# Kernel tuning notes

Hardware: AMD Instinct MI355X
Metric: run time of the kernel (lower is better)

## Reference

```python
import jax, jax.numpy as jnp
import numpy as np

V, CV, F, E, H, A, CD = 10000, 64, 2048, 512, 512, 512, 128
B, LCAP = 128, 31  # 30 decode steps


def setup_inputs() -> dict:
    key = jax.random.key(0)
    ks = jax.random.split(key, 24)
    g = lambda k, shp, s: (jax.random.normal(k, shp, jnp.float32) * s)
    return {
        "att_feats": g(ks[0], (B, F, 7, 7), 1.0),
        "fc_feats": g(ks[1], (B, F), 1.0),
        "captions": jax.random.randint(ks[2], (B, LCAP), 0, V),
        "count_vecs": g(ks[3], (B, CV), 1.0),
        "embed_w": jax.random.uniform(ks[4], (V, E), jnp.float32, -0.1, 0.1),
        "cm_w1": g(ks[5], (CD, CV), 0.05), "cm_b1": jnp.zeros((CD,), jnp.float32),
        "cm_w2": g(ks[6], (CD, CD), 0.05), "cm_b2": jnp.zeros((CD,), jnp.float32),
        "att_hw": g(ks[7], (A, H), 0.03), "att_hb": jnp.zeros((A,), jnp.float32),
        "att_fw": g(ks[8], (A, F), 0.02), "att_fb": jnp.zeros((A,), jnp.float32),
        "alpha_w": g(ks[9], (1, A), 0.03), "alpha_b": jnp.zeros((1,), jnp.float32),
        "fcproj_w": g(ks[10], (H, F), 0.02), "fcproj_b": jnp.zeros((H,), jnp.float32),
        "w_ih": g(ks[11], (4 * H, E + F + CD), 0.02), "b_ih": jnp.zeros((4 * H,), jnp.float32),
        "w_hh": g(ks[12], (4 * H, H), 0.03), "b_hh": jnp.zeros((4 * H,), jnp.float32),
        "fc_w": jax.random.uniform(ks[13], (V, H), jnp.float32, -0.1, 0.1),
        "fc_b": jnp.zeros((V,), jnp.float32),
    }


def reference(att_feats, fc_feats, captions, count_vecs,
              embed_w, cm_w1, cm_b1, cm_w2, cm_b2,
              att_hw, att_hb, att_fw, att_fb, alpha_w, alpha_b,
              fcproj_w, fcproj_b, w_ih, b_ih, w_hh, b_hh, fc_w, fc_b):
    # Eval-mode forward with teacher forcing (dropout = identity).
    b = att_feats.shape[0]
    att = att_feats.reshape(b, F, -1).transpose(0, 2, 1)  # [B,49,F]
    count_embed = jax.nn.relu(count_vecs @ cm_w1.T + cm_b1) @ cm_w2.T + cm_b2  # [B,CD]
    h0 = jnp.tanh(fc_feats @ fcproj_w.T + fcproj_b)  # [B,H]
    c0 = jnp.zeros_like(h0)
    att_proj = att @ att_fw.T + att_fb  # [B,49,A] (hoisted: time-invariant)
    word_embeds = embed_w[captions[:, :-1]]  # [B,T,E]

    def step(carry, we_t):
        h, c = carry
        hp = h @ att_hw.T + att_hb                       # [B,A]
        comb = jnp.tanh(att_proj + hp[:, None, :])       # [B,49,A]
        scores = comb @ alpha_w[0] + alpha_b[0]          # [B,49]
        alpha = jax.nn.softmax(scores, axis=1)
        context = jnp.einsum('bn,bnf->bf', alpha, att)   # [B,F]
        x = jnp.concatenate([we_t, context, count_embed], axis=1)
        gates = x @ w_ih.T + b_ih + h @ w_hh.T + b_hh    # [B,4H]
        i, f, g, o = jnp.split(gates, 4, axis=1)
        c_new = jax.nn.sigmoid(f) * c + jax.nn.sigmoid(i) * jnp.tanh(g)
        h_new = jax.nn.sigmoid(o) * jnp.tanh(c_new)
        logits = h_new @ fc_w.T + fc_b                   # [B,V]
        return (h_new, c_new), (logits, alpha)

    (_, _), (outs, alphas) = jax.lax.scan(step, (h0, c0), word_embeds.transpose(1, 0, 2))
    return outs.transpose(1, 0, 2), alphas.transpose(1, 0, 2)  # [B,T,V], [B,T,49]
```

## Files before the change

kernel.cpp:

```cpp
#include <hip/hip_runtime.h>
#include <cstdint>

#define B_   128
#define T_   30
#define F_   2048
#define E_   512
#define H_   512
#define A_   512
#define CD_  128
#define CV_  64
#define V_   10000
#define VP_  10112
#define NN_  49
#define G4_  2048
#define LCAP_ 31

typedef __attribute__((ext_vector_type(4))) float f32x4;
typedef _Float16 h2v __attribute__((ext_vector_type(2)));
typedef _Float16 h4v __attribute__((ext_vector_type(4)));
typedef _Float16 h8v __attribute__((ext_vector_type(8)));

__device__ __forceinline__ float fdot2f(h2v a, h2v b, float c) {
#if __has_builtin(__builtin_amdgcn_fdot2)
  return __builtin_amdgcn_fdot2(a, b, c, false);
#else
  return c + (float)a[0]*(float)b[0] + (float)a[1]*(float)b[1];
#endif
}
__device__ __forceinline__ float dot8(h8v x, h8v w, float acc) {
  acc = fdot2f((h2v){x[0],x[1]}, (h2v){w[0],w[1]}, acc);
  acc = fdot2f((h2v){x[2],x[3]}, (h2v){w[2],w[3]}, acc);
  acc = fdot2f((h2v){x[4],x[5]}, (h2v){w[4],w[5]}, acc);
  acc = fdot2f((h2v){x[6],x[7]}, (h2v){w[6],w[7]}, acc);
  return acc;
}
__device__ __forceinline__ float tanh_f(float x) {
  x = fminf(fmaxf(x, -15.f), 15.f);
  float e = __expf(2.f * x);
  return __fdividef(e - 1.f, e + 1.f);
}
__device__ __forceinline__ float sig_f(float x) {
  return __fdividef(1.f, 1.f + __expf(-x));
}

template<int OUT_H, int BIAS>
__global__ __launch_bounds__(256)
void gemm_h16(const _Float16* __restrict__ A, int lda,
              const _Float16* __restrict__ B, int ldb,
              const float* __restrict__ bias,
              void* __restrict__ Cv, int ldc, int Nreal, int K) {
  __shared__ _Float16 As[128 * 32];
  __shared__ _Float16 Bs[128 * 32];
  const int tid = threadIdx.x;
  const int m0 = blockIdx.y * 128, n0 = blockIdx.x * 128;
  const int lane = tid & 63, wid = tid >> 6;
  const int wm = (wid >> 1) * 64, wn = (wid & 1) * 64;
  f32x4 acc[4][4] = {};
  const int lr = tid >> 2;
  const int lc = (tid & 3) * 8;
  const _Float16* Ag  = A + (size_t)(m0 + lr) * lda + lc;
  const _Float16* Ag2 = Ag + (size_t)64 * lda;
  const _Float16* Bg  = B + (size_t)(n0 + lr) * ldb + lc;
  const _Float16* Bg2 = Bg + (size_t)64 * ldb;
  auto* lAs = (__attribute__((address_space(3))) char*)As;
  auto* lBs = (__attribute__((address_space(3))) char*)Bs;
  const int ldst = lr * 64 + (tid & 3) * 16;
  const int ar = wm + (lane & 15);
  const int br = wn + (lane & 15);
  const int kc = (lane >> 4) * 8;
  for (int k0 = 0; k0 < K; k0 += 32) {
    __builtin_amdgcn_global_load_lds((const __attribute__((address_space(1))) char*)(Ag  + k0), lAs + ldst,        16, 0, 0);
    __builtin_amdgcn_global_load_lds((const __attribute__((address_space(1))) char*)(Ag2 + k0), lAs + 4096 + ldst, 16, 0, 0);
    __builtin_amdgcn_global_load_lds((const __attribute__((address_space(1))) char*)(Bg  + k0), lBs + ldst,        16, 0, 0);
    __builtin_amdgcn_global_load_lds((const __attribute__((address_space(1))) char*)(Bg2 + k0), lBs + 4096 + ldst, 16, 0, 0);
    __syncthreads();
    h8v af[4], bfr[4];
#pragma unroll
    for (int i = 0; i < 4; ++i) {
      af[i]  = *(const h8v*)&As[(ar + i * 16) * 32 + kc];
      bfr[i] = *(const h8v*)&Bs[(br + i * 16) * 32 + kc];
    }
#pragma unroll
    for (int i = 0; i < 4; ++i)
#pragma unroll
      for (int j = 0; j < 4; ++j)
        acc[i][j] = __builtin_amdgcn_mfma_f32_16x16x32_f16(af[i], bfr[j], acc[i][j], 0, 0, 0);
    __syncthreads();
  }
  const int orow = m0 + wm + (lane >> 4) * 4;
  const int ocol = n0 + wn + (lane & 15);
#pragma unroll
  for (int j = 0; j < 4; ++j) {
    const int col = ocol + j * 16;
    if (col >= Nreal) continue;
    const float bv = BIAS ? bias[col] : 0.f;
#pragma unroll
    for (int i = 0; i < 4; ++i) {
#pragma unroll
      for (int r = 0; r < 4; ++r) {
        const int row = orow + i * 16 + r;
        const float v = acc[i][j][r] + bv;
        if (OUT_H) ((_Float16*)Cv)[(size_t)row * ldc + col] = (_Float16)v;
        else       ((float*)Cv)[(size_t)row * ldc + col] = v;
      }
    }
  }
}

__global__ __launch_bounds__(256)
void transpose_att(const float* __restrict__ af, _Float16* __restrict__ att_th) {
  __shared__ float s[64 * NN_];
  const int b = blockIdx.y, f0 = blockIdx.x * 64;
  const float* src = af + (size_t)b * F_ * NN_ + (size_t)f0 * NN_;
  for (int i = threadIdx.x; i < 64 * NN_; i += 256) s[i] = src[i];
  __syncthreads();
  _Float16* dst = att_th + (size_t)b * NN_ * F_ + f0;
  for (int i = threadIdx.x; i < NN_ * 64; i += 256) {
    int n = i >> 6, j = i & 63;
    dst[(size_t)n * F_ + j] = (_Float16)s[j * NN_ + n];
  }
}

__global__ void pack_h16(const float* __restrict__ src, int src_ld, int c0,
                         _Float16* __restrict__ dst, int C, int R, int Rpad) {
  int i = blockIdx.x * 256 + threadIdx.x;
  if (i >= Rpad * C) return;
  int r = i / C, c = i - r * C;
  float v = (r < R) ? src[(size_t)r * src_ld + c0 + c] : 0.f;
  dst[i] = (_Float16)v;
}

__global__ void pack_ki8(const float* __restrict__ src, int src_ld, int c0,
                         _Float16* __restrict__ dst, int R, int K) {
  int i = blockIdx.x * 256 + threadIdx.x;
  if (i >= R * K) return;
  int k7 = i & 7;
  int t = i >> 3;
  int r = t & (R - 1);
  int kb = t / R;
  int k = kb * 8 + k7;
  dst[i] = (_Float16)src[(size_t)r * src_ld + c0 + k];
}

__global__ __launch_bounds__(128)
void count_embed_k(const float* __restrict__ cv, const float* __restrict__ w1,
                   const float* __restrict__ b1, const float* __restrict__ w2,
                   const float* __restrict__ b2, float* __restrict__ ce) {
  const int b = blockIdx.x, tid = threadIdx.x;
  __shared__ float s_cv[CV_], s_h[CD_];
  if (tid < CV_) s_cv[tid] = cv[b * CV_ + tid];
  __syncthreads();
  float acc = b1[tid];
  for (int k = 0; k < CV_; ++k) acc += s_cv[k] * w1[tid * CV_ + k];
  s_h[tid] = fmaxf(acc, 0.f);
  __syncthreads();
  float acc2 = b2[tid];
  for (int k = 0; k < CD_; ++k) acc2 += s_h[k] * w2[tid * CD_ + k];
  ce[b * CD_ + tid] = acc2;
}

__global__ __launch_bounds__(128)
void gather_we(const int* __restrict__ captions, const float* __restrict__ embed_w,
               _Float16* __restrict__ we_h) {
  const int r = blockIdx.x;
  const int b = r / T_, t = r - b * T_;
  const int idx = captions[b * LCAP_ + t];
  const float4 v = ((const float4*)(embed_w + (size_t)idx * E_))[threadIdx.x];
  h4v o = { (_Float16)v.x, (_Float16)v.y, (_Float16)v.z, (_Float16)v.w };
  ((h4v*)(we_h + (size_t)r * E_))[threadIdx.x] = o;
}

__global__ __launch_bounds__(1024)
void seq_loop(const _Float16* __restrict__ fcfeat_h,
              const _Float16* __restrict__ fcproj_k,
              const float* __restrict__ fcproj_b,
              const _Float16* __restrict__ wcnt_h,
              const float* __restrict__ ce,
              const float* __restrict__ b_ih, const float* __restrict__ b_hh,
              const _Float16* __restrict__ atthw_k,
              const float* __restrict__ att_hb,
              const _Float16* __restrict__ attproj_h,
              const float* __restrict__ alpha_w, const float* __restrict__ alpha_b,
              const _Float16* __restrict__ attW_h,
              const float* __restrict__ we_proj,
              const _Float16* __restrict__ whh_k,
              _Float16* __restrict__ H_all_h,
              float* __restrict__ out_alpha) {
  const int b = blockIdx.x, tid = threadIdx.x;
  __shared__ _Float16 s_ap[NN_ * A_];
  __shared__ _Float16 s_h[H_];
  __shared__ float    s_hp2[2][A_];
  __shared__ _Float16 s_gates[G4_];
  __shared__ float    s_sc[64];
  __shared__ float    s_alpha[64];
  __shared__ float    s_ce[CD_];

  const int a9 = tid & 511, half = tid >> 9;
  const int wv = tid >> 6, lane = tid & 63;

  ((uint*)s_gates)[tid] = ((const uint*)(fcfeat_h + (size_t)b * F_))[tid];
  {
    const uint* src = (const uint*)(attproj_h + (size_t)b * NN_ * A_);
    for (int i = tid; i < NN_ * A_ / 2; i += 1024) ((uint*)s_ap)[i] = src[i];
  }
  if (tid < CD_) s_ce[tid] = ce[b * CD_ + tid];
  h2v aW[NN_];
  {
    const _Float16* base = attW_h + (size_t)b * NN_ * G4_ + 2 * tid;
#pragma unroll
    for (int n = 0; n < NN_; ++n) aW[n] = *(const h2v*)(base + (size_t)n * G4_);
  }
  float aw8[8];
#pragma unroll
  for (int i = 0; i < 8; ++i) aw8[i] = alpha_w[lane * 8 + i];
  const float ab  = alpha_b[0];
  const float ahb = (half == 0) ? att_hb[a9] : 0.f;
  __syncthreads();

  float c_state = 0.f;
  if (tid < H_) {
    float acc = fcproj_b[tid];
    const h8v* xv = (const h8v*)s_gates;
    const h8v* wp = (const h8v*)fcproj_k;
    for (int k8 = 0; k8 < F_ / 8; ++k8)
      acc = dot8(xv[k8], wp[(size_t)k8 * 512 + tid], acc);
    s_h[tid] = (_Float16)tanh_f(acc);
  }
  float base0 = b_ih[2 * tid]     + b_hh[2 * tid];
  float base1 = b_ih[2 * tid + 1] + b_hh[2 * tid + 1];
  {
    const h8v* w0 = (const h8v*)(wcnt_h + (size_t)(2 * tid) * CD_);
    const h8v* w1 = (const h8v*)(wcnt_h + (size_t)(2 * tid + 1) * CD_);
#pragma unroll
    for (int k8 = 0; k8 < CD_ / 8; ++k8) {
      const h8v a = w0[k8], c = w1[k8];
#pragma unroll
      for (int i = 0; i < 8; ++i) {
        const float cv = s_ce[k8 * 8 + i];
        base0 += cv * (float)a[i];
        base1 += cv * (float)c[i];
      }
    }
  }
  __syncthreads();

  const h8v* atthw8 = (const h8v*)atthw_k;
  const h8v* whh8   = (const h8v*)whh_k;

  for (int t = 0; t < T_; ++t) {
    {
      float acc = ahb;
      const h8v* hv = (const h8v*)s_h;
      const int k80 = half * 32;
#pragma unroll 8
      for (int k8 = k80; k8 < k80 + 32; ++k8)
        acc = dot8(hv[k8], atthw8[(size_t)k8 * 512 + a9], acc);
      s_hp2[half][a9] = acc;
    }
    __syncthreads();
    {
      float hp8[8];
#pragma unroll
      for (int i = 0; i < 8; ++i) {
        const int a = lane * 8 + i;
        hp8[i] = s_hp2[0][a] + s_hp2[1][a];
      }
      const int Q = (wv == 0) ? 4 : 3;
      for (int q = 0; q < Q; ++q) {
        const int n = wv + 16 * q;
        const h8v apv = *(const h8v*)&s_ap[n * A_ + lane * 8];
        float s = 0.f;
#pragma unroll
        for (int i = 0; i < 8; ++i) {
          const float x = (float)apv[i] + hp8[i];
          const float e = __expf(2.f * fminf(fmaxf(x, -15.f), 15.f));
          s += __fdividef(e - 1.f, e + 1.f) * aw8[i];
        }
#pragma unroll
        for (int off = 32; off > 0; off >>= 1) s += __shfl_xor(s, off);
        if (lane == 0) s_sc[n] = s + ab;
      }
    }
    __syncthreads();
    if (wv == 0) {
      float v = (lane < NN_) ? s_sc[lane] : -3.0e38f;
      float m = v;
#pragma unroll
      for (int off = 32; off > 0; off >>= 1) m = fmaxf(m, __shfl_xor(m, off));
      float e = (lane < NN_) ? __expf(v - m) : 0.f;
      float ssum = e;
#pragma unroll
      for (int off = 32; off > 0; off >>= 1) ssum += __shfl_xor(ssum, off);
      const float a = __fdividef(e, ssum);
      if (lane < NN_) {
        s_alpha[lane] = a;
        out_alpha[((size_t)b * T_ + t) * NN_ + lane] = a;
      }
    }
    __syncthreads();
    {
      const float2 wp = *(const float2*)(we_proj + ((size_t)b * T_ + t) * G4_ + 2 * tid);
      float acc0 = base0 + wp.x, acc1 = base1 + wp.y;
#pragma unroll
      for (int n = 0; n < NN_; ++n) {
        const float al = s_alpha[n];
        acc0 += al * (float)aW[n][0];
        acc1 += al * (float)aW[n][1];
      }
      const h8v* hv = (const h8v*)s_h;
#pragma unroll 4
      for (int k8 = 0; k8 < H_ / 8; ++k8) {
        const h8v x = hv[k8];
        acc0 = dot8(x, whh8[(size_t)k8 * G4_ + 2 * tid],     acc0);
        acc1 = dot8(x, whh8[(size_t)k8 * G4_ + 2 * tid + 1], acc1);
      }
      *(h2v*)&s_gates[2 * tid] = (h2v){ (_Float16)acc0, (_Float16)acc1 };
    }
    __syncthreads();
    if (tid < H_) {
      const int j = tid;
      const float gi = (float)s_gates[j];
      const float gf = (float)s_gates[512 + j];
      const float gg = (float)s_gates[1024 + j];
      const float go = (float)s_gates[1536 + j];
      const float si = sig_f(gi), sf = sig_f(gf), so = sig_f(go);
      c_state = sf * c_state + si * tanh_f(gg);
      const float hn = so * tanh_f(c_state);
      s_h[j] = (_Float16)hn;
      H_all_h[((size_t)b * T_ + t) * H_ + j] = (_Float16)hn;
    }
    __syncthreads();
  }
}

extern "C" void kernel_launch(void* const* d_in, const int* in_sizes, int n_in,
                              void* d_out, int out_size, void* d_ws, size_t ws_size,
                              hipStream_t stream) {
  const float* att_feats  = (const float*)d_in[0];
  const float* fc_feats   = (const float*)d_in[1];
  const int*   captions   = (const int*)  d_in[2];
  const float* count_vecs = (const float*)d_in[3];
  const float* embed_w    = (const float*)d_in[4];
  const float* cm_w1      = (const float*)d_in[5];
  const float* cm_b1      = (const float*)d_in[6];
  const float* cm_w2      = (const float*)d_in[7];
  const float* cm_b2      = (const float*)d_in[8];
  const float* att_hw     = (const float*)d_in[9];
  const float* att_hb     = (const float*)d_in[10];
  const float* att_fw     = (const float*)d_in[11];
  const float* att_fb     = (const float*)d_in[12];
  const float* alpha_w    = (const float*)d_in[13];
  const float* alpha_b    = (const float*)d_in[14];
  const float* fcproj_w   = (const float*)d_in[15];
  const float* fcproj_b   = (const float*)d_in[16];
  const float* w_ih       = (const float*)d_in[17];
  const float* b_ih       = (const float*)d_in[18];
  const float* w_hh       = (const float*)d_in[19];
  const float* b_hh       = (const float*)d_in[20];
  const float* fc_w       = (const float*)d_in[21];
  const float* fc_b       = (const float*)d_in[22];
  float* out = (float*)d_out;

  char* wsb = (char*)d_ws;
  size_t off = 0;
  auto nxt = [&](size_t bytes) { char* p = wsb + off; off += (bytes + 255) & ~(size_t)255; return p; };
  _Float16* att_th    = (_Float16*)nxt((size_t)B_*NN_*F_*2);
  _Float16* attW_h    = (_Float16*)nxt((size_t)B_*NN_*G4_*2);
  _Float16* attproj_h = (_Float16*)nxt((size_t)B_*NN_*A_*2);
  _Float16* we_h      = (_Float16*)nxt((size_t)B_*T_*E_*2);
  _Float16* H_all_h   = (_Float16*)nxt((size_t)B_*T_*H_*2);
  _Float16* w_ihF_h   = (_Float16*)nxt((size_t)G4_*F_*2);
  _Float16* w_ih0_h   = (_Float16*)nxt((size_t)G4_*E_*2);
  _Float16* wcnt_h    = (_Float16*)nxt((size_t)G4_*CD_*2);
  _Float16* fc_w_h    = (_Float16*)nxt((size_t)VP_*H_*2);
  _Float16* att_fw_h  = (_Float16*)nxt((size_t)A_*F_*2);
  _Float16* fcfeat_h  = (_Float16*)nxt((size_t)B_*F_*2);
  _Float16* whh_k     = (_Float16*)nxt((size_t)G4_*H_*2);
  _Float16* atthw_k   = (_Float16*)nxt((size_t)A_*H_*2);
  _Float16* fcproj_k  = (_Float16*)nxt((size_t)H_*F_*2);
  float*    we_proj   = (float*)nxt((size_t)B_*T_*G4_*4);
  float*    ce        = (float*)nxt((size_t)B_*CD_*4);
  if (off > ws_size) return;

  const size_t ALPHA_OFF = (size_t)B_ * T_ * V_;

  transpose_att<<<dim3(F_/64, B_), 256, 0, stream>>>(att_feats, att_th);
  pack_h16<<<((size_t)B_*F_ + 255)/256, 256, 0, stream>>>(fc_feats, F_, 0, fcfeat_h, F_, B_, B_);
  pack_h16<<<((size_t)G4_*F_ + 255)/256, 256, 0, stream>>>(w_ih, E_+F_+CD_, E_, w_ihF_h, F_, G4_, G4_);
  pack_h16<<<((size_t)G4_*E_ + 255)/256, 256, 0, stream>>>(w_ih, E_+F_+CD_, 0, w_ih0_h, E_, G4_, G4_);
  pack_h16<<<((size_t)G4_*CD_ + 255)/256, 256, 0, stream>>>(w_ih, E_+F_+CD_, E_+F_, wcnt_h, CD_, G4_, G4_);
  pack_h16<<<((size_t)A_*F_ + 255)/256, 256, 0, stream>>>(att_fw, F_, 0, att_fw_h, F_, A_, A_);
  pack_h16<<<((size_t)VP_*H_ + 255)/256, 256, 0, stream>>>(fc_w, H_, 0, fc_w_h, H_, V_, VP_);
  pack_ki8<<<((size_t)G4_*H_ + 255)/256, 256, 0, stream>>>(w_hh, H_, 0, whh_k, G4_, H_);
  pack_ki8<<<((size_t)A_*H_ + 255)/256, 256, 0, stream>>>(att_hw, H_, 0, atthw_k, A_, H_);
  pack_ki8<<<((size_t)H_*F_ + 255)/256, 256, 0, stream>>>(fcproj_w, F_, 0, fcproj_k, H_, F_);
  count_embed_k<<<B_, 128, 0, stream>>>(count_vecs, cm_w1, cm_b1, cm_w2, cm_b2, ce);
  gather_we<<<B_ * T_, 128, 0, stream>>>(captions, embed_w, we_h);

  gemm_h16<1,1><<<dim3(A_/128, (B_*NN_)/128), 256, 0, stream>>>(
      att_th, F_, att_fw_h, F_, att_fb, attproj_h, A_, A_, F_);
  gemm_h16<1,0><<<dim3(G4_/128, (B_*NN_)/128), 256, 0, stream>>>(
      att_th, F_, w_ihF_h, F_, nullptr, attW_h, G4_, G4_, F_);
  gemm_h16<0,0><<<dim3(G4_/128, (B_*T_)/128), 256, 0, stream>>>(
      we_h, E_, w_ih0_h, E_, nullptr, we_proj, G4_, G4_, E_);

  seq_loop<<<B_, 1024, 0, stream>>>(fcfeat_h, fcproj_k, fcproj_b,
                                    wcnt_h, ce, b_ih, b_hh,
                                    atthw_k, att_hb,
                                    attproj_h, alpha_w, alpha_b,
                                    attW_h, we_proj, whh_k,
                                    H_all_h, out + ALPHA_OFF);

  gemm_h16<0,1><<<dim3(VP_/128, (B_*T_)/128), 256, 0, stream>>>(
      H_all_h, H_, fc_w_h, H_, fc_b, out, V_, V_, H_);
}
```

Baseline: 1.840 ms.

## Split recurrent loop across 256 persistent blocks with grid barriers

The sequential LSTM-attention loop was one block per batch row, so each block streamed all recurrent weights every step. It now runs as a persistent kernel of 256 blocks, each owning a slice of hidden units and keeping its slice of w_hh and att_hw in LDS. Hidden state, attention projections and alphas are exchanged through global memory with three atomic grid barriers per step. The count-embedding and fc-projection preprocessing move into separate GEMMs, and GEMM outputs are written directly in the per-block layouts. This adds barrier latency and relies on all 256 blocks being co-resident, otherwise the spin barrier can deadlock.

```diff
diff --git a/kernel.cpp b/kernel.cpp
--- a/kernel.cpp
+++ b/kernel.cpp
@@ -14,10 +14,11 @@
 #define NN_  49
 #define G4_  2048
 #define LCAP_ 31
+#define NBLK_ 256
+#define NTH_  512
 
 typedef __attribute__((ext_vector_type(4))) float f32x4;
 typedef _Float16 h2v __attribute__((ext_vector_type(2)));
-typedef _Float16 h4v __attribute__((ext_vector_type(4)));
 typedef _Float16 h8v __attribute__((ext_vector_type(8)));
 
 __device__ __forceinline__ float fdot2f(h2v a, h2v b, float c) {
@@ -27,13 +28,6 @@
   return c + (float)a[0]*(float)b[0] + (float)a[1]*(float)b[1];
 #endif
 }
-__device__ __forceinline__ float dot8(h8v x, h8v w, float acc) {
-  acc = fdot2f((h2v){x[0],x[1]}, (h2v){w[0],w[1]}, acc);
-  acc = fdot2f((h2v){x[2],x[3]}, (h2v){w[2],w[3]}, acc);
-  acc = fdot2f((h2v){x[4],x[5]}, (h2v){w[4],w[5]}, acc);
-  acc = fdot2f((h2v){x[6],x[7]}, (h2v){w[6],w[7]}, acc);
-  return acc;
-}
 __device__ __forceinline__ float tanh_f(float x) {
   x = fminf(fmaxf(x, -15.f), 15.f);
   float e = __expf(2.f * x);
@@ -43,7 +37,7 @@
   return __fdividef(1.f, 1.f + __expf(-x));
 }
 
-template<int OUT_H, int BIAS>
+template<int OMODE, int BIAS>
 __global__ __launch_bounds__(256)
 void gemm_h16(const _Float16* __restrict__ A, int lda,
               const _Float16* __restrict__ B, int ldb,
@@ -92,7 +86,7 @@
 #pragma unroll
   for (int j = 0; j < 4; ++j) {
     const int col = ocol + j * 16;
-    if (col >= Nreal) continue;
+    if ((OMODE == 0 || OMODE == 1 || OMODE == 4) && col >= Nreal) continue;
     const float bv = BIAS ? bias[col] : 0.f;
 #pragma unroll
     for (int i = 0; i < 4; ++i) {
@@ -100,9 +94,77 @@
       for (int r = 0; r < 4; ++r) {
         const int row = orow + i * 16 + r;
         const float v = acc[i][j][r] + bv;
-        if (OUT_H) ((_Float16*)Cv)[(size_t)row * ldc + col] = (_Float16)v;
-        else       ((float*)Cv)[(size_t)row * ldc + col] = v;
-      }
+        if (OMODE == 0) {
+          ((float*)Cv)[(size_t)row * ldc + col] = v;
+        } else if (OMODE == 1) {
+          ((_Float16*)Cv)[(size_t)row * ldc + col] = (_Float16)v;
+        } else if (OMODE == 4) {
+          ((_Float16*)Cv)[(size_t)row * ldc + col] = (_Float16)tanh_f(v);
+        } else if (OMODE == 2) {
+          const int b = row / NN_, n = row - b * NN_;
+          const int q = col >> 9, rem = col & 511, gg = rem >> 1, jl = rem & 1;
+          ((_Float16*)Cv)[((((size_t)gg * B_ + b) * NN_ + n) << 3) + q * 2 + jl] = (_Float16)v;
+        } else if (OMODE == 3) {
+          const int b = row / T_, tt = row - b * T_;
+          const int q = col >> 9, rem = col & 511, gg = rem >> 1, jl = rem & 1;
+          ((_Float16*)Cv)[((((size_t)gg * T_ + tt) * B_ + b) << 3) + q * 2 + jl] = (_Float16)v;
+        }
+      }
+    }
+  }
+}
+
+template<int ACT>
+__global__ __launch_bounds__(256)
+void gemm_nt(const float* __restrict__ A, int lda,
+             const float* __restrict__ Bt, int ldb,
+             const float* __restrict__ bias,
+             float* __restrict__ C, int ldc,
+             int M, int N, int K) {
+  __shared__ float As[16][64];
+  __shared__ float Bs[16][64];
+  const int tid = threadIdx.x;
+  const int tx = tid & 15, ty = tid >> 4;
+  const int n0 = blockIdx.x * 64, m0 = blockIdx.y * 64;
+  const int lrow = tid >> 2, lkq = (tid & 3) << 2;
+  const bool aval = (m0 + lrow) < M;
+  const bool bval = (n0 + lrow) < N;
+  const float* Ap = A  + (size_t)(m0 + lrow) * lda + lkq;
+  const float* Bp = Bt + (size_t)(n0 + lrow) * ldb + lkq;
+  float acc[4][4] = {};
+  for (int k0 = 0; k0 < K; k0 += 16) {
+    float4 av = make_float4(0.f,0.f,0.f,0.f), bv = make_float4(0.f,0.f,0.f,0.f);
+    if (aval) av = *(const float4*)(Ap + k0);
+    if (bval) bv = *(const float4*)(Bp + k0);
+    __syncthreads();
+    As[lkq+0][lrow]=av.x; As[lkq+1][lrow]=av.y; As[lkq+2][lrow]=av.z; As[lkq+3][lrow]=av.w;
+    Bs[lkq+0][lrow]=bv.x; Bs[lkq+1][lrow]=bv.y; Bs[lkq+2][lrow]=bv.z; Bs[lkq+3][lrow]=bv.w;
+    __syncthreads();
+#pragma unroll
+    for (int k = 0; k < 16; ++k) {
+      float a4[4], b4[4];
+#pragma unroll
+      for (int i = 0; i < 4; ++i) a4[i] = As[k][ty*4+i];
+#pragma unroll
+      for (int j = 0; j < 4; ++j) b4[j] = Bs[k][tx*4+j];
+#pragma unroll
+      for (int i = 0; i < 4; ++i)
+#pragma unroll
+        for (int j = 0; j < 4; ++j) acc[i][j] += a4[i]*b4[j];
+    }
+  }
+#pragma unroll
+  for (int i = 0; i < 4; ++i) {
+    int m = m0 + ty*4 + i;
+    if (m >= M) continue;
+#pragma unroll
+    for (int j = 0; j < 4; ++j) {
+      int n = n0 + tx*4 + j;
+      if (n >= N) continue;
+      float v = acc[i][j];
+      if (bias) v += bias[n];
+      if (ACT == 1) v = tanhf(v);
+      C[(size_t)m * ldc + n] = v;
     }
   }
 }
@@ -130,16 +192,18 @@
   dst[i] = (_Float16)v;
 }
 
-__global__ void pack_ki8(const float* __restrict__ src, int src_ld, int c0,
-                         _Float16* __restrict__ dst, int R, int K) {
+__global__ void repack_whh(const float* __restrict__ w_hh, _Float16* __restrict__ whhr) {
   int i = blockIdx.x * 256 + threadIdx.x;
-  if (i >= R * K) return;
-  int k7 = i & 7;
-  int t = i >> 3;
-  int r = t & (R - 1);
-  int kb = t / R;
-  int k = kb * 8 + k7;
-  dst[i] = (_Float16)src[(size_t)r * src_ld + c0 + k];
+  if (i >= 256 * 8 * 512) return;
+  int k = i & 511, p = (i >> 9) & 7, g = i >> 12;
+  int q = p >> 1, jl = p & 1;
+  whhr[i] = (_Float16)w_hh[(size_t)(q * 512 + 2 * g + jl) * H_ + k];
+}
+__global__ void repack_wa(const float* __restrict__ att_hw, _Float16* __restrict__ wa_r) {
+  int i = blockIdx.x * 256 + threadIdx.x;
+  if (i >= 256 * 2 * 512) return;
+  int k = i & 511, a1 = (i >> 9) & 1, g = i >> 10;
+  wa_r[i] = (_Float16)att_hw[(size_t)(2 * g + a1) * H_ + k];
 }
 
 __global__ __launch_bounds__(128)
@@ -166,113 +230,133 @@
   const int b = r / T_, t = r - b * T_;
   const int idx = captions[b * LCAP_ + t];
   const float4 v = ((const float4*)(embed_w + (size_t)idx * E_))[threadIdx.x];
-  h4v o = { (_Float16)v.x, (_Float16)v.y, (_Float16)v.z, (_Float16)v.w };
-  ((h4v*)(we_h + (size_t)r * E_))[threadIdx.x] = o;
-}
-
-__global__ __launch_bounds__(1024)
-void seq_loop(const _Float16* __restrict__ fcfeat_h,
-              const _Float16* __restrict__ fcproj_k,
-              const float* __restrict__ fcproj_b,
-              const _Float16* __restrict__ wcnt_h,
-              const float* __restrict__ ce,
-              const float* __restrict__ b_ih, const float* __restrict__ b_hh,
-              const _Float16* __restrict__ atthw_k,
+  _Float16 o[4] = {(_Float16)v.x, (_Float16)v.y, (_Float16)v.z, (_Float16)v.w};
+  *(h2v*)(we_h + (size_t)r * E_ + threadIdx.x * 4)     = *(h2v*)&o[0];
+  *(h2v*)(we_h + (size_t)r * E_ + threadIdx.x * 4 + 2) = *(h2v*)&o[2];
+}
+
+__global__ void addvec_k(const float* __restrict__ a, const float* __restrict__ b,
+                         float* __restrict__ o, int n) {
+  int i = blockIdx.x * 256 + threadIdx.x;
+  if (i < n) o[i] = a[i] + b[i];
+}
+__global__ void zero_k(float* __restrict__ p, int n) {
+  int i = blockIdx.x * 256 + threadIdx.x;
+  if (i < n) p[i] = 0.f;
+}
+
+#define OFF_AP   0
+#define OFF_HS   50176
+#define OFF_WHH  83072
+#define OFF_WA   91264
+#define OFF_PACC 93312
+#define OFF_BASE 109696
+#define OFF_GACC 113792
+#define OFF_HP   117888
+#define OFF_CS   119936
+#define OFF_SC   120960
+#define OFF_AL   121216
+#define SEQ_LDS  121472
+
+__device__ __forceinline__ void gridbar(unsigned* bar, int& gen) {
+  __syncthreads();
+  if (threadIdx.x == 0) {
+    __threadfence();
+    __hip_atomic_fetch_add(bar, 1u, __ATOMIC_RELAXED, __HIP_MEMORY_SCOPE_AGENT);
+    const unsigned target = (unsigned)(++gen) * (unsigned)NBLK_;
+    while (__hip_atomic_load(bar, __ATOMIC_RELAXED, __HIP_MEMORY_SCOPE_AGENT) < target)
+      __builtin_amdgcn_s_sleep(2);
+    __threadfence();
+  }
+  __syncthreads();
+}
+
+__global__ __launch_bounds__(NTH_)
+void seq_loop(const _Float16* __restrict__ whhr,
+              const _Float16* __restrict__ wa_r,
+              const float* __restrict__ base_glob,
+              const _Float16* __restrict__ attproj,
+              const float* __restrict__ alpha_w, const float* __restrict__ alpha_b,
               const float* __restrict__ att_hb,
-              const _Float16* __restrict__ attproj_h,
-              const float* __restrict__ alpha_w, const float* __restrict__ alpha_b,
-              const _Float16* __restrict__ attW_h,
-              const float* __restrict__ we_proj,
-              const _Float16* __restrict__ whh_k,
-              _Float16* __restrict__ H_all_h,
-              float* __restrict__ out_alpha) {
-  const int b = blockIdx.x, tid = threadIdx.x;
-  __shared__ _Float16 s_ap[NN_ * A_];
-  __shared__ _Float16 s_h[H_];
-  __shared__ float    s_hp2[2][A_];
-  __shared__ _Float16 s_gates[G4_];
-  __shared__ float    s_sc[64];
-  __shared__ float    s_alpha[64];
-  __shared__ float    s_ce[CD_];
-
-  const int a9 = tid & 511, half = tid >> 9;
-  const int wv = tid >> 6, lane = tid & 63;
-
-  ((uint*)s_gates)[tid] = ((const uint*)(fcfeat_h + (size_t)b * F_))[tid];
-  {
-    const uint* src = (const uint*)(attproj_h + (size_t)b * NN_ * A_);
-    for (int i = tid; i < NN_ * A_ / 2; i += 1024) ((uint*)s_ap)[i] = src[i];
-  }
-  if (tid < CD_) s_ce[tid] = ce[b * CD_ + tid];
-  h2v aW[NN_];
-  {
-    const _Float16* base = attW_h + (size_t)b * NN_ * G4_ + 2 * tid;
-#pragma unroll
-    for (int n = 0; n < NN_; ++n) aW[n] = *(const h2v*)(base + (size_t)n * G4_);
+              const _Float16* __restrict__ attWr,
+              const _Float16* __restrict__ wepr,
+              _Float16* __restrict__ h_glob,
+              float* __restrict__ hp_glob,
+              float* __restrict__ alpha_glob,
+              _Float16* __restrict__ H_all,
+              float* __restrict__ out_alpha,
+              unsigned* __restrict__ bar) {
+  extern __shared__ char smem[];
+  _Float16* ap_s  = (_Float16*)(smem + OFF_AP);
+  _Float16* h_s   = (_Float16*)(smem + OFF_HS);
+  _Float16* whh_s = (_Float16*)(smem + OFF_WHH);
+  _Float16* wa_s  = (_Float16*)(smem + OFF_WA);
+  float* pacc   = (float*)(smem + OFF_PACC);
+  float* base_s = (float*)(smem + OFF_BASE);
+  float* gacc   = (float*)(smem + OFF_GACC);
+  float* s_hp   = (float*)(smem + OFF_HP);
+  float* c_s    = (float*)(smem + OFF_CS);
+  float* s_sc   = (float*)(smem + OFF_SC);
+
+  const int g = blockIdx.x, tid = threadIdx.x;
+  const int lane = tid & 63, wv = tid >> 6;
+
+  if (tid < 512) ((h8v*)whh_s)[tid] = ((const h8v*)(whhr + (size_t)g * 8 * 512))[tid];
+  if (tid < 128) ((h8v*)wa_s)[tid]  = ((const h8v*)(wa_r + (size_t)g * 2 * 512))[tid];
+  for (int it = tid; it < 1024; it += NTH_) {
+    const int p = it & 7, b = it >> 3;
+    const int q = p >> 1, jl = p & 1;
+    base_s[p * 128 + b] = base_glob[(size_t)b * G4_ + q * 512 + 2 * g + jl];
+  }
+  if (tid < 256) c_s[tid] = 0.f;
+  if (g < B_) {
+    const h8v* src = (const h8v*)(attproj + (size_t)g * NN_ * A_);
+    for (int i = tid; i < NN_ * A_ / 8; i += NTH_) ((h8v*)ap_s)[i] = src[i];
   }
   float aw8[8];
 #pragma unroll
-  for (int i = 0; i < 8; ++i) aw8[i] = alpha_w[lane * 8 + i];
+  for (int i = 0; i < 8; ++i) aw8[i] = alpha_w[lane + 64 * i];
   const float ab  = alpha_b[0];
-  const float ahb = (half == 0) ? att_hb[a9] : 0.f;
+  const float ahb = att_hb[2 * g + (tid >> 8)];
   __syncthreads();
-
-  float c_state = 0.f;
-  if (tid < H_) {
-    float acc = fcproj_b[tid];
-    const h8v* xv = (const h8v*)s_gates;
-    const h8v* wp = (const h8v*)fcproj_k;
-    for (int k8 = 0; k8 < F_ / 8; ++k8)
-      acc = dot8(xv[k8], wp[(size_t)k8 * 512 + tid], acc);
-    s_h[tid] = (_Float16)tanh_f(acc);
-  }
-  float base0 = b_ih[2 * tid]     + b_hh[2 * tid];
-  float base1 = b_ih[2 * tid + 1] + b_hh[2 * tid + 1];
-  {
-    const h8v* w0 = (const h8v*)(wcnt_h + (size_t)(2 * tid) * CD_);
-    const h8v* w1 = (const h8v*)(wcnt_h + (size_t)(2 * tid + 1) * CD_);
-#pragma unroll
-    for (int k8 = 0; k8 < CD_ / 8; ++k8) {
-      const h8v a = w0[k8], c = w1[k8];
-#pragma unroll
-      for (int i = 0; i < 8; ++i) {
-        const float cv = s_ce[k8 * 8 + i];
-        base0 += cv * (float)a[i];
-        base1 += cv * (float)c[i];
-      }
-    }
-  }
-  __syncthreads();
-
-  const h8v* atthw8 = (const h8v*)atthw_k;
-  const h8v* whh8   = (const h8v*)whh_k;
+  int gen = 0;
 
   for (int t = 0; t < T_; ++t) {
+    const _Float16* h_rd = h_glob + (size_t)(t & 1) * (B_ * H_);
+    _Float16* h_wr = h_glob + (size_t)((t + 1) & 1) * (B_ * H_);
     {
-      float acc = ahb;
-      const h8v* hv = (const h8v*)s_h;
-      const int k80 = half * 32;
-#pragma unroll 8
-      for (int k8 = k80; k8 < k80 + 32; ++k8)
-        acc = dot8(hv[k8], atthw8[(size_t)k8 * 512 + a9], acc);
-      s_hp2[half][a9] = acc;
-    }
-    __syncthreads();
-    {
-      float hp8[8];
-#pragma unroll
-      for (int i = 0; i < 8; ++i) {
-        const int a = lane * 8 + i;
-        hp8[i] = s_hp2[0][a] + s_hp2[1][a];
-      }
-      const int Q = (wv == 0) ? 4 : 3;
-      for (int q = 0; q < Q; ++q) {
-        const int n = wv + 16 * q;
-        const h8v apv = *(const h8v*)&s_ap[n * A_ + lane * 8];
+      const int k8 = tid & 7, b5 = (tid >> 3) & 31, a1 = tid >> 8;
+      for (int c = 0; c < 4; ++c) {
+        __syncthreads();
+        const uint* src = (const uint*)(h_rd + (size_t)c * 32 * H_);
+#pragma unroll
+        for (int i = 0; i < 16; ++i) {
+          const int m = tid + i * NTH_;
+          ((uint*)h_s)[(m >> 8) * 257 + (m & 255)] = src[m];
+        }
+        __syncthreads();
+        float acc = 0.f;
+        const h2v* hrow = (const h2v*)(h_s + b5 * 514);
+        const h2v* wrow = (const h2v*)(wa_s + a1 * 512);
+#pragma unroll
+        for (int kk = 0; kk < 32; ++kk)
+          acc = fdot2f(hrow[k8 * 32 + kk], wrow[k8 * 32 + kk], acc);
+        acc += __shfl_xor(acc, 1);
+        acc += __shfl_xor(acc, 2);
+        acc += __shfl_xor(acc, 4);
+        if (k8 == 0) hp_glob[(size_t)(c * 32 + b5) * A_ + 2 * g + a1] = acc + ahb;
+      }
+    }
+    gridbar(bar, gen);
+    if (g < B_) {
+      if (tid < A_) s_hp[tid] = hp_glob[(size_t)g * A_ + tid];
+      __syncthreads();
+      for (int n = wv; n < NN_; n += 8) {
         float s = 0.f;
 #pragma unroll
         for (int i = 0; i < 8; ++i) {
-          const float x = (float)apv[i] + hp8[i];
+          const int a = lane + 64 * i;
+          const float x = (float)ap_s[n * A_ + a] + s_hp[a];
           const float e = __expf(2.f * fminf(fmaxf(x, -15.f), 15.f));
           s += __fdividef(e - 1.f, e + 1.f) * aw8[i];
         }
@@ -280,56 +364,90 @@
         for (int off = 32; off > 0; off >>= 1) s += __shfl_xor(s, off);
         if (lane == 0) s_sc[n] = s + ab;
       }
-    }
-    __syncthreads();
-    if (wv == 0) {
-      float v = (lane < NN_) ? s_sc[lane] : -3.0e38f;
-      float m = v;
-#pragma unroll
-      for (int off = 32; off > 0; off >>= 1) m = fmaxf(m, __shfl_xor(m, off));
-      float e = (lane < NN_) ? __expf(v - m) : 0.f;
-      float ssum = e;
-#pragma unroll
-      for (int off = 32; off > 0; off >>= 1) ssum += __shfl_xor(ssum, off);
-      const float a = __fdividef(e, ssum);
-      if (lane < NN_) {
-        s_alpha[lane] = a;
-        out_alpha[((size_t)b * T_ + t) * NN_ + lane] = a;
-      }
-    }
-    __syncthreads();
+      __syncthreads();
+      if (wv == 0) {
+        float v = (lane < NN_) ? s_sc[lane] : -3.0e38f;
+        float m = v;
+#pragma unroll
+        for (int off = 32; off > 0; off >>= 1) m = fmaxf(m, __shfl_xor(m, off));
+        float e = (lane < NN_) ? __expf(v - m) : 0.f;
+        float ssum = e;
+#pragma unroll
+        for (int off = 32; off > 0; off >>= 1) ssum += __shfl_xor(ssum, off);
+        const float a = __fdividef(e, ssum);
+        if (lane < NN_) {
+          alpha_glob[(size_t)g * 64 + lane] = a;
+          out_alpha[((size_t)g * T_ + t) * NN_ + lane] = a;
+        }
+      }
+    }
+    gridbar(bar, gen);
     {
-      const float2 wp = *(const float2*)(we_proj + ((size_t)b * T_ + t) * G4_ + 2 * tid);
-      float acc0 = base0 + wp.x, acc1 = base1 + wp.y;
-#pragma unroll
-      for (int n = 0; n < NN_; ++n) {
-        const float al = s_alpha[n];
-        acc0 += al * (float)aW[n][0];
-        acc1 += al * (float)aW[n][1];
-      }
-      const h8v* hv = (const h8v*)s_h;
-#pragma unroll 4
-      for (int k8 = 0; k8 < H_ / 8; ++k8) {
-        const h8v x = hv[k8];
-        acc0 = dot8(x, whh8[(size_t)k8 * G4_ + 2 * tid],     acc0);
-        acc1 = dot8(x, whh8[(size_t)k8 * G4_ + 2 * tid + 1], acc1);
-      }
-      *(h2v*)&s_gates[2 * tid] = (h2v){ (_Float16)acc0, (_Float16)acc1 };
-    }
-    __syncthreads();
-    if (tid < H_) {
-      const int j = tid;
-      const float gi = (float)s_gates[j];
-      const float gf = (float)s_gates[512 + j];
-      const float gg = (float)s_gates[1024 + j];
-      const float go = (float)s_gates[1536 + j];
+      const int nq = tid & 3, b = tid >> 2;
+      f32x4 p0 = {0,0,0,0}, p1 = {0,0,0,0};
+      const float* arow = alpha_glob + (size_t)b * 64;
+      const _Float16* wrow = attWr + (((size_t)g * B_ + b) * NN_) * 8;
+      for (int n = nq; n < NN_; n += 4) {
+        const float al = arow[n];
+        const h8v w = *(const h8v*)(wrow + (size_t)n * 8);
+#pragma unroll
+        for (int i = 0; i < 4; ++i) { p0[i] += al * (float)w[i]; p1[i] += al * (float)w[4+i]; }
+      }
+      float* pr = pacc + ((size_t)b * 4 + nq) * 8;
+      *(f32x4*)pr = p0; *(f32x4*)(pr + 4) = p1;
+    }
+    __syncthreads();
+    {
+      const _Float16* wep = wepr + (((size_t)g * T_ + t) * B_) * 8;
+#pragma unroll
+      for (int e = 0; e < 2; ++e) {
+        const int item = tid * 2 + e;
+        const int p = item & 7, b = item >> 3;
+        float s = base_s[p * 128 + b] + (float)wep[(size_t)b * 8 + p];
+        const float* pr = pacc + (size_t)b * 32 + p;
+#pragma unroll
+        for (int nq = 0; nq < 4; ++nq) s += pr[nq * 8];
+        gacc[p * 128 + b] = s;
+      }
+    }
+    __syncthreads();
+    {
+      const int kh = tid & 1, b5 = (tid >> 1) & 31, p3 = tid >> 6;
+      for (int c = 0; c < 4; ++c) {
+        __syncthreads();
+        const uint* src = (const uint*)(h_rd + (size_t)c * 32 * H_);
+#pragma unroll
+        for (int i = 0; i < 16; ++i) {
+          const int m = tid + i * NTH_;
+          ((uint*)h_s)[(m >> 8) * 257 + (m & 255)] = src[m];
+        }
+        __syncthreads();
+        float acc = 0.f;
+        const h2v* hrow = (const h2v*)(h_s + b5 * 514);
+        const h2v* wrow = (const h2v*)(whh_s + p3 * 512);
+#pragma unroll 16
+        for (int kk = 0; kk < 128; ++kk)
+          acc = fdot2f(hrow[kh * 128 + kk], wrow[kh * 128 + kk], acc);
+        acc += __shfl_xor(acc, 1);
+        if (kh == 0) gacc[p3 * 128 + c * 32 + b5] += acc;
+      }
+    }
+    __syncthreads();
+    if (tid < 256) {
+      const int jl = tid & 1, b = tid >> 1;
+      const float gi = gacc[(0 + jl) * 128 + b];
+      const float gf = gacc[(2 + jl) * 128 + b];
+      const float gg = gacc[(4 + jl) * 128 + b];
+      const float go = gacc[(6 + jl) * 128 + b];
       const float si = sig_f(gi), sf = sig_f(gf), so = sig_f(go);
-      c_state = sf * c_state + si * tanh_f(gg);
-      const float hn = so * tanh_f(c_state);
-      s_h[j] = (_Float16)hn;
-      H_all_h[((size_t)b * T_ + t) * H_ + j] = (_Float16)hn;
-    }
-    __syncthreads();
+      float c = c_s[jl * 128 + b];
+      c = sf * c + si * tanh_f(gg);
+      c_s[jl * 128 + b] = c;
+      const float hn = so * tanh_f(c);
+      h_wr[(size_t)b * H_ + 2 * g + jl] = (_Float16)hn;
+      H_all[((size_t)b * T_ + t) * H_ + 2 * g + jl] = (_Float16)hn;
+    }
+    gridbar(bar, gen);
   }
 }
 
@@ -365,51 +483,60 @@
   size_t off = 0;
   auto nxt = [&](size_t bytes) { char* p = wsb + off; off += (bytes + 255) & ~(size_t)255; return p; };
   _Float16* att_th    = (_Float16*)nxt((size_t)B_*NN_*F_*2);
-  _Float16* attW_h    = (_Float16*)nxt((size_t)B_*NN_*G4_*2);
   _Float16* attproj_h = (_Float16*)nxt((size_t)B_*NN_*A_*2);
   _Float16* we_h      = (_Float16*)nxt((size_t)B_*T_*E_*2);
   _Float16* H_all_h   = (_Float16*)nxt((size_t)B_*T_*H_*2);
   _Float16* w_ihF_h   = (_Float16*)nxt((size_t)G4_*F_*2);
   _Float16* w_ih0_h   = (_Float16*)nxt((size_t)G4_*E_*2);
-  _Float16* wcnt_h    = (_Float16*)nxt((size_t)G4_*CD_*2);
   _Float16* fc_w_h    = (_Float16*)nxt((size_t)VP_*H_*2);
   _Float16* att_fw_h  = (_Float16*)nxt((size_t)A_*F_*2);
   _Float16* fcfeat_h  = (_Float16*)nxt((size_t)B_*F_*2);
-  _Float16* whh_k     = (_Float16*)nxt((size_t)G4_*H_*2);
-  _Float16* atthw_k   = (_Float16*)nxt((size_t)A_*H_*2);
-  _Float16* fcproj_k  = (_Float16*)nxt((size_t)H_*F_*2);
-  float*    we_proj   = (float*)nxt((size_t)B_*T_*G4_*4);
+  _Float16* fcproj_h  = (_Float16*)nxt((size_t)H_*F_*2);
+  _Float16* attWr     = (_Float16*)nxt((size_t)256*B_*NN_*8*2);
+  _Float16* wepr      = (_Float16*)nxt((size_t)256*T_*B_*8*2);
+  _Float16* whhr      = (_Float16*)nxt((size_t)256*8*512*2);
+  _Float16* wa_r      = (_Float16*)nxt((size_t)256*2*512*2);
+  _Float16* h_glob    = (_Float16*)nxt((size_t)2*B_*H_*2);
   float*    ce        = (float*)nxt((size_t)B_*CD_*4);
+  float*    bsum      = (float*)nxt((size_t)G4_*4);
+  float*    base_glob = (float*)nxt((size_t)B_*G4_*4);
+  float*    hp_glob   = (float*)nxt((size_t)B_*A_*4);
+  float*    alpha_g   = (float*)nxt((size_t)B_*64*4);
+  unsigned* bar       = (unsigned*)nxt(256);
   if (off > ws_size) return;
 
   const size_t ALPHA_OFF = (size_t)B_ * T_ * V_;
 
   transpose_att<<<dim3(F_/64, B_), 256, 0, stream>>>(att_feats, att_th);
   pack_h16<<<((size_t)B_*F_ + 255)/256, 256, 0, stream>>>(fc_feats, F_, 0, fcfeat_h, F_, B_, B_);
+  pack_h16<<<((size_t)H_*F_ + 255)/256, 256, 0, stream>>>(fcproj_w, F_, 0, fcproj_h, F_, H_, H_);
   pack_h16<<<((size_t)G4_*F_ + 255)/256, 256, 0, stream>>>(w_ih, E_+F_+CD_, E_, w_ihF_h, F_, G4_, G4_);
   pack_h16<<<((size_t)G4_*E_ + 255)/256, 256, 0, stream>>>(w_ih, E_+F_+CD_, 0, w_ih0_h, E_, G4_, G4_);
-  pack_h16<<<((size_t)G4_*CD_ + 255)/256, 256, 0, stream>>>(w_ih, E_+F_+CD_, E_+F_, wcnt_h, CD_, G4_, G4_);
   pack_h16<<<((size_t)A_*F_ + 255)/256, 256, 0, stream>>>(att_fw, F_, 0, att_fw_h, F_, A_, A_);
   pack_h16<<<((size_t)VP_*H_ + 255)/256, 256, 0, stream>>>(fc_w, H_, 0, fc_w_h, H_, V_, VP_);
-  pack_ki8<<<((size_t)G4_*H_ + 255)/256, 256, 0, stream>>>(w_hh, H_, 0, whh_k, G4_, H_);
-  pack_ki8<<<((size_t)A_*H_ + 255)/256, 256, 0, stream>>>(att_hw, H_, 0, atthw_k, A_, H_);
-  pack_ki8<<<((size_t)H_*F_ + 255)/256, 256, 0, stream>>>(fcproj_w, F_, 0, fcproj_k, H_, F_);
+  repack_whh<<<(256*8*512 + 255)/256, 256, 0, stream>>>(w_hh, whhr);
+  repack_wa<<<(256*2*512 + 255)/256, 256, 0, stream>>>(att_hw, wa_r);
   count_embed_k<<<B_, 128, 0, stream>>>(count_vecs, cm_w1, cm_b1, cm_w2, cm_b2, ce);
+  addvec_k<<<(G4_ + 255)/256, 256, 0, stream>>>(b_ih, b_hh, bsum, G4_);
   gather_we<<<B_ * T_, 128, 0, stream>>>(captions, embed_w, we_h);
-
+  zero_k<<<1, 64, 0, stream>>>((float*)bar, 64);
+
+  gemm_nt<0><<<dim3(G4_/64, B_/64), 256, 0, stream>>>(ce, CD_, w_ih + E_ + F_, E_+F_+CD_,
+                                                      bsum, base_glob, G4_, B_, G4_, CD_);
   gemm_h16<1,1><<<dim3(A_/128, (B_*NN_)/128), 256, 0, stream>>>(
       att_th, F_, att_fw_h, F_, att_fb, attproj_h, A_, A_, F_);
-  gemm_h16<1,0><<<dim3(G4_/128, (B_*NN_)/128), 256, 0, stream>>>(
-      att_th, F_, w_ihF_h, F_, nullptr, attW_h, G4_, G4_, F_);
-  gemm_h16<0,0><<<dim3(G4_/128, (B_*T_)/128), 256, 0, stream>>>(
-      we_h, E_, w_ih0_h, E_, nullptr, we_proj, G4_, G4_, E_);
-
-  seq_loop<<<B_, 1024, 0, stream>>>(fcfeat_h, fcproj_k, fcproj_b,
-                                    wcnt_h, ce, b_ih, b_hh,
-                                    atthw_k, att_hb,
-                                    attproj_h, alpha_w, alpha_b,
-                                    attW_h, we_proj, whh_k,
-                                    H_all_h, out + ALPHA_OFF);
+  gemm_h16<2,0><<<dim3(G4_/128, (B_*NN_)/128), 256, 0, stream>>>(
+      att_th, F_, w_ihF_h, F_, nullptr, attWr, G4_, G4_, F_);
+  gemm_h16<3,0><<<dim3(G4_/128, (B_*T_)/128), 256, 0, stream>>>(
+      we_h, E_, w_ih0_h, E_, nullptr, wepr, G4_, G4_, E_);
+  gemm_h16<4,1><<<dim3(H_/128, B_/128), 256, 0, stream>>>(
+      fcfeat_h, F_, fcproj_h, F_, fcproj_b, h_glob, H_, H_, F_);
+
+  hipFuncSetAttribute((const void*)seq_loop, hipFuncAttributeMaxDynamicSharedMemorySize, SEQ_LDS);
+  seq_loop<<<NBLK_, NTH_, SEQ_LDS, stream>>>(whhr, wa_r, base_glob, attproj_h,
+                                             alpha_w, alpha_b, att_hb,
+                                             attWr, wepr, h_glob, hp_glob, alpha_g,
+                                             H_all_h, out + ALPHA_OFF, bar);
 
   gemm_h16<0,1><<<dim3(VP_/128, (B_*T_)/128), 256, 0, stream>>>(
       H_all_h, H_, fc_w_h, H_, fc_b, out, V_, V_, H_);
```

Result: slower. 3.391 ms (+84.3%).
